# Optimization experiments

Measured on AMD Instinct MI355X. Metric: run time of the kernel, lower is better.

The kernel has to match this reference:

```python
import jax, jax.numpy as jnp
import numpy as np

K, DIM, B, N_CLASS = 4096, 50257, 512, 2


def setup_inputs() -> dict:
    key = jax.random.key(0)
    k1, k2, k3 = jax.random.split(key, 3)
    # probability-like positive values; log() is applied to both tensors
    query = jax.random.uniform(k1, (B, DIM), dtype=jnp.float32, minval=1e-4, maxval=1.0)
    queue_anchor = jax.random.uniform(k2, (K, DIM), dtype=jnp.float32, minval=1e-4, maxval=1.0)
    queue_label = jax.random.randint(k3, (K,), 0, N_CLASS, dtype=jnp.int64)
    return {"query": query, "queue_anchor": queue_anchor, "queue_label": queue_label}


def reference(query, queue_anchor, queue_label):
    # Original math: kl[b,k] = mean_d( a[k,d] * (log a[k,d] - log q[b,d]) )
    # Decompose to avoid the (K,B,dim) broadcast:
    #   kl = mean_d(a*log a)[k] - (a @ log(q).T)[k,b] / dim
    a = queue_anchor
    dim = a.shape[1]
    ent = jnp.mean(a * jnp.log(a), axis=1)                    # (K,)
    cross = jnp.einsum('kd,bd->kb', a, jnp.log(query)) / dim  # (K,B)
    kl_distance = (ent[:, None] - cross).T                    # (B,K)
    # knn == 1 path: argmin over anchors, gather labels
    indices = jnp.argmin(kl_distance, axis=1)                 # (B,)
    return queue_label[indices]
```

## Files before the change

kernel.cpp:

```cpp
#include <hip/hip_runtime.h>
#include <stdint.h>

#define DIMN 50257
#define KN   4096
#define BN   512
#define DP   50432
#define DCH  6304
#define NSTAGE 197
#define MARGIN_RAW 6.0f

#define OFF_CROSS 0ul
#define OFF_ENT   8388608ul
#define OFF_CNT   8404992ul
#define OFF_CANDK 8407040ul
#define OFF_CANDV 8439808ul
#define OFF_LQ16  8472576ul

typedef short v8s __attribute__((ext_vector_type(8)));
typedef float v4f __attribute__((ext_vector_type(4)));

__device__ __forceinline__ unsigned short bf16_rne(float x) {
    unsigned u = __float_as_uint(x);
    u += 0x7fffu + ((u >> 16) & 1u);
    return (unsigned short)(u >> 16);
}

__global__ void k_zero(float* __restrict__ p, long n) {
    long i = (long)blockIdx.x * blockDim.x + threadIdx.x;
    long stride = (long)gridDim.x * blockDim.x;
    for (; i < n; i += stride) p[i] = 0.0f;
}

__global__ void k_logq(const float* __restrict__ q, unsigned short* __restrict__ lq) {
    long i = (long)blockIdx.x * 256 + threadIdx.x;
    if (i >= (long)BN * DP) return;
    int b = (int)(i / DP);
    int d = (int)(i - (long)b * DP);
    unsigned short h = 0;
    if (d < DIMN) {
        float x = q[(long)b * DIMN + d];
        h = bf16_rne(__logf(x));
    }
    lq[i] = h;
}

__global__ __launch_bounds__(512, 2) void k_gemm(
    const float* __restrict__ A, const unsigned short* __restrict__ LQ,
    float* __restrict__ cross, float* __restrict__ ent)
{
    __shared__ __align__(16) unsigned short a_s[128 * 40];
    __shared__ __align__(16) unsigned short b_s[512 * 40];

    const int t    = threadIdx.x;
    const int bid  = blockIdx.x;
    const int rt   = bid >> 3;
    const int ch   = bid & 7;
    const int k0   = rt * 128;
    const int dbase = ch * DCH;

    const int lane = t & 63;
    const int w    = t >> 6;
    const int wr   = w >> 2;
    const int wc   = w & 3;
    const int aq   = lane >> 4;
    const int am   = lane & 15;

    const int ac  = t & 31;
    const int ar0 = t >> 5;
    const int bn0  = t >> 2;
    const int bsub = t & 3;

    v4f acc[4][8];
#pragma unroll
    for (int i = 0; i < 4; ++i)
#pragma unroll
        for (int j = 0; j < 8; ++j) acc[i][j] = (v4f){0.f, 0.f, 0.f, 0.f};

    float ent_acc[8];
#pragma unroll
    for (int i = 0; i < 8; ++i) ent_acc[i] = 0.f;

    int abase[8];
#pragma unroll
    for (int i = 0; i < 8; ++i) abase[i] = (k0 + ar0 + 16 * i) * DIMN + dbase + ac;
    int bbase[4];
#pragma unroll
    for (int i = 0; i < 4; ++i) bbase[i] = (bn0 + 128 * i) * DP + dbase + bsub * 8;

    float a_reg[8];
    v8s   b_reg[4];

    {
        const int d = dbase + ac;
#pragma unroll
        for (int i = 0; i < 8; ++i)
            a_reg[i] = (d < DIMN) ? A[abase[i]] : 0.0f;
#pragma unroll
        for (int i = 0; i < 4; ++i)
            b_reg[i] = *(const v8s*)&LQ[bbase[i]];
    }

#pragma unroll 1
    for (int s = 0; s < NSTAGE; ++s) {
        __syncthreads();
#pragma unroll
        for (int i = 0; i < 8; ++i) {
            float av = a_reg[i];
            if (av > 0.f) ent_acc[i] += av * __logf(av);
            a_s[(ar0 + 16 * i) * 40 + ac] = bf16_rne(av);
        }
#pragma unroll
        for (int i = 0; i < 4; ++i)
            *(v8s*)&b_s[(bn0 + 128 * i) * 40 + bsub * 8] = b_reg[i];
        __syncthreads();

        if (s + 1 < NSTAGE) {
            const int off = (s + 1) * 32;
            const int d = dbase + off + ac;
#pragma unroll
            for (int i = 0; i < 8; ++i)
                a_reg[i] = (d < DIMN) ? A[abase[i] + off] : 0.0f;
#pragma unroll
            for (int i = 0; i < 4; ++i)
                b_reg[i] = *(const v8s*)&LQ[bbase[i] + off];
        }

        v8s aF[4], bF[8];
#pragma unroll
        for (int i = 0; i < 4; ++i)
            aF[i] = *(const v8s*)&a_s[(wr * 64 + i * 16 + am) * 40 + aq * 8];
#pragma unroll
        for (int j = 0; j < 8; ++j)
            bF[j] = *(const v8s*)&b_s[(wc * 128 + j * 16 + am) * 40 + aq * 8];
#pragma unroll
        for (int i = 0; i < 4; ++i)
#pragma unroll
            for (int j = 0; j < 8; ++j)
                acc[i][j] = __builtin_amdgcn_mfma_f32_16x16x32_bf16(aF[i], bF[j], acc[i][j], 0, 0, 0);
    }

#pragma unroll
    for (int i = 0; i < 4; ++i)
#pragma unroll
        for (int j = 0; j < 8; ++j)
#pragma unroll
            for (int r = 0; r < 4; ++r) {
                int row = k0 + wr * 64 + i * 16 + aq * 4 + r;
                int col = wc * 128 + j * 16 + am;
                atomicAdd(&cross[(long)row * BN + col], acc[i][j][r]);
            }
#pragma unroll
    for (int i = 0; i < 8; ++i) {
        float v = ent_acc[i];
#pragma unroll
        for (int m = 1; m <= 16; m <<= 1) v += __shfl_xor(v, m, 64);
        if ((lane & 31) == 0) atomicAdd(&ent[k0 + ar0 + 16 * i], v);
    }
}

__global__ void k_argmin(const float* __restrict__ cross, const float* __restrict__ ent,
                         int* __restrict__ cnt, int* __restrict__ candk)
{
    __shared__ float sred[256];
    __shared__ int scnt;
    const int b = blockIdx.x;
    const int t = threadIdx.x;
    float vals[16];
    float best = 3.4e38f;
#pragma unroll
    for (int i = 0; i < 16; ++i) {
        int k = t + i * 256;
        float v = ent[k] - cross[(long)k * BN + b];
        vals[i] = v;
        best = fminf(best, v);
    }
    sred[t] = best;
    __syncthreads();
    for (int o = 128; o > 0; o >>= 1) {
        if (t < o) sred[t] = fminf(sred[t], sred[t + o]);
        __syncthreads();
    }
    if (t == 0) scnt = 0;
    __syncthreads();
    const float m1 = sred[0];
#pragma unroll
    for (int i = 0; i < 16; ++i) {
        if (vals[i] <= m1 + MARGIN_RAW) {
            int pos = atomicAdd(&scnt, 1);
            if (pos < 16) candk[b * 16 + pos] = t + i * 256;
        }
    }
    __syncthreads();
    if (t == 0) cnt[b] = min(scnt, 16);
}

__global__ void k_refine(const float* __restrict__ A, const float* __restrict__ q,
                         const float* __restrict__ ent, const int* __restrict__ cnt,
                         const int* __restrict__ candk, float* __restrict__ candv)
{
    __shared__ double sred[256];
    const int b = blockIdx.x >> 4;
    const int j = blockIdx.x & 15;
    if (j >= cnt[b]) return;
    const int k = candk[b * 16 + j];
    const int t = threadIdx.x;
    const float* __restrict__ arow = A + (long)k * DIMN;
    const float* __restrict__ qrow = q + (long)b * DIMN;
    double sum = 0.0;
    for (int d = t; d < DIMN; d += 256)
        sum += (double)arow[d] * (double)__logf(qrow[d]);
    sred[t] = sum;
    __syncthreads();
    for (int o = 128; o > 0; o >>= 1) {
        if (t < o) sred[t] += sred[t + o];
        __syncthreads();
    }
    if (t == 0) candv[b * 16 + j] = (float)((double)ent[k] - sred[0]);
}

__global__ void k_final(const float* __restrict__ candv, const int* __restrict__ candk,
                        const int* __restrict__ cnt, const int* __restrict__ label,
                        int* __restrict__ out)
{
    int b = blockIdx.x * blockDim.x + threadIdx.x;
    if (b >= BN) return;
    int n = cnt[b];
    float bv = 3.4e38f;
    int bk = 1 << 30;
    for (int j = 0; j < n; ++j) {
        float v = candv[b * 16 + j];
        int kk = candk[b * 16 + j];
        if (v < bv || (v == bv && kk < bk)) { bv = v; bk = kk; }
    }
    out[b] = label[bk];
}

extern "C" void kernel_launch(void* const* d_in, const int* in_sizes, int n_in,
                              void* d_out, int out_size, void* d_ws, size_t ws_size,
                              hipStream_t stream)
{
    const float* q     = (const float*)d_in[0];
    const float* A     = (const float*)d_in[1];
    const int*   label = (const int*)d_in[2];
    int* out = (int*)d_out;

    char* ws = (char*)d_ws;
    float*          cross = (float*)(ws + OFF_CROSS);
    float*          ent   = (float*)(ws + OFF_ENT);
    int*            cnt   = (int*)(ws + OFF_CNT);
    int*            candk = (int*)(ws + OFF_CANDK);
    float*          candv = (float*)(ws + OFF_CANDV);
    unsigned short* lq    = (unsigned short*)(ws + OFF_LQ16);

    k_zero<<<1024, 256, 0, stream>>>((float*)ws, (long)(OFF_CANDK / 4));
    k_logq<<<(int)(((long)BN * DP + 255) / 256), 256, 0, stream>>>(q, lq);
    k_gemm<<<256, 512, 0, stream>>>(A, lq, cross, ent);
    k_argmin<<<BN, 256, 0, stream>>>(cross, ent, cnt, candk);
    k_refine<<<BN * 16, 256, 0, stream>>>(A, q, ent, cnt, candk, candv);
    k_final<<<2, 256, 0, stream>>>(candv, candk, cnt, label, out);
}
```

Measured before the change: 1.855 ms.

## Use direct global-to-LDS loads, split-D partial buffers, and vectorize logq/refine

```diff
diff --git a/kernel.cpp b/kernel.cpp
--- a/kernel.cpp
+++ b/kernel.cpp
@@ -7,17 +7,19 @@
 #define DP   50432
 #define DCH  6304
 #define NSTAGE 197
+#define NCH  8
 #define MARGIN_RAW 6.0f
 
 #define OFF_CROSS 0ul
-#define OFF_ENT   8388608ul
-#define OFF_CNT   8404992ul
-#define OFF_CANDK 8407040ul
-#define OFF_CANDV 8439808ul
-#define OFF_LQ16  8472576ul
+#define OFF_ENT   67108864ul
+#define OFF_CNT   67125248ul
+#define OFF_CANDK 67127296ul
+#define OFF_CANDV 67160064ul
+#define OFF_LQ16  67192832ul
 
 typedef short v8s __attribute__((ext_vector_type(8)));
 typedef float v4f __attribute__((ext_vector_type(4)));
+typedef unsigned short v4su __attribute__((ext_vector_type(4)));
 
 __device__ __forceinline__ unsigned short bf16_rne(float x) {
     unsigned u = __float_as_uint(x);
@@ -25,23 +27,37 @@
     return (unsigned short)(u >> 16);
 }
 
-__global__ void k_zero(float* __restrict__ p, long n) {
-    long i = (long)blockIdx.x * blockDim.x + threadIdx.x;
-    long stride = (long)gridDim.x * blockDim.x;
-    for (; i < n; i += stride) p[i] = 0.0f;
+__device__ __forceinline__ void lds_load16(const unsigned short* g, unsigned short* l) {
+    __builtin_amdgcn_global_load_lds(
+        reinterpret_cast<const unsigned int __attribute__((address_space(1)))*>(
+            reinterpret_cast<uintptr_t>(g)),
+        reinterpret_cast<unsigned int __attribute__((address_space(3)))*>(
+            reinterpret_cast<uintptr_t>(l)),
+        16, 0, 0);
+}
+
+__global__ void k_zero(float* __restrict__ p, int n) {
+    int i = blockIdx.x * 256 + threadIdx.x;
+    if (i < n) p[i] = 0.0f;
 }
 
 __global__ void k_logq(const float* __restrict__ q, unsigned short* __restrict__ lq) {
-    long i = (long)blockIdx.x * 256 + threadIdx.x;
-    if (i >= (long)BN * DP) return;
-    int b = (int)(i / DP);
-    int d = (int)(i - (long)b * DP);
-    unsigned short h = 0;
-    if (d < DIMN) {
-        float x = q[(long)b * DIMN + d];
-        h = bf16_rne(__logf(x));
-    }
-    lq[i] = h;
+    const int b  = blockIdx.y;
+    const int d0 = (blockIdx.x * 256 + threadIdx.x) * 4;
+    if (d0 >= DP) return;
+    const float* __restrict__ qr = q + (long)b * DIMN;
+    v4su out;
+    if (d0 + 3 < DIMN) {
+#pragma unroll
+        for (int i = 0; i < 4; ++i) out[i] = bf16_rne(__logf(qr[d0 + i]));
+    } else {
+#pragma unroll
+        for (int i = 0; i < 4; ++i) {
+            int d = d0 + i;
+            out[i] = (d < DIMN) ? bf16_rne(__logf(qr[d])) : (unsigned short)0;
+        }
+    }
+    *(v4su*)(lq + (long)b * DP + d0) = out;
 }
 
 __global__ __launch_bounds__(512, 2) void k_gemm(
@@ -49,13 +65,12 @@
     float* __restrict__ cross, float* __restrict__ ent)
 {
     __shared__ __align__(16) unsigned short a_s[128 * 40];
-    __shared__ __align__(16) unsigned short b_s[512 * 40];
-
-    const int t    = threadIdx.x;
-    const int bid  = blockIdx.x;
-    const int rt   = bid >> 3;
-    const int ch   = bid & 7;
-    const int k0   = rt * 128;
+    __shared__ __align__(16) unsigned short b_s[2][512 * 32];
+
+    const int t     = threadIdx.x;
+    const int rt    = blockIdx.x >> 3;
+    const int ch    = blockIdx.x & 7;
+    const int k0    = rt * 128;
     const int dbase = ch * DCH;
 
     const int lane = t & 63;
@@ -67,8 +82,8 @@
 
     const int ac  = t & 31;
     const int ar0 = t >> 5;
-    const int bn0  = t >> 2;
-    const int bsub = t & 3;
+    const int brow = w * 64 + (lane >> 2);
+    const int bcol = (lane & 3) * 8;
 
     v4f acc[4][8];
 #pragma unroll
@@ -83,12 +98,8 @@
     int abase[8];
 #pragma unroll
     for (int i = 0; i < 8; ++i) abase[i] = (k0 + ar0 + 16 * i) * DIMN + dbase + ac;
-    int bbase[4];
-#pragma unroll
-    for (int i = 0; i < 4; ++i) bbase[i] = (bn0 + 128 * i) * DP + dbase + bsub * 8;
 
     float a_reg[8];
-    v8s   b_reg[4];
 
     {
         const int d = dbase + ac;
@@ -96,8 +107,9 @@
         for (int i = 0; i < 8; ++i)
             a_reg[i] = (d < DIMN) ? A[abase[i]] : 0.0f;
 #pragma unroll
-        for (int i = 0; i < 4; ++i)
-            b_reg[i] = *(const v8s*)&LQ[bbase[i]];
+        for (int n = 0; n < 4; ++n)
+            lds_load16(LQ + (brow + n * 16) * DP + dbase + bcol,
+                       &b_s[0][w * 2048 + n * 512]);
     }
 
 #pragma unroll 1
@@ -109,9 +121,6 @@
             if (av > 0.f) ent_acc[i] += av * __logf(av);
             a_s[(ar0 + 16 * i) * 40 + ac] = bf16_rne(av);
         }
-#pragma unroll
-        for (int i = 0; i < 4; ++i)
-            *(v8s*)&b_s[(bn0 + 128 * i) * 40 + bsub * 8] = b_reg[i];
         __syncthreads();
 
         if (s + 1 < NSTAGE) {
@@ -121,24 +130,25 @@
             for (int i = 0; i < 8; ++i)
                 a_reg[i] = (d < DIMN) ? A[abase[i] + off] : 0.0f;
 #pragma unroll
-            for (int i = 0; i < 4; ++i)
-                b_reg[i] = *(const v8s*)&LQ[bbase[i] + off];
-        }
-
-        v8s aF[4], bF[8];
+            for (int n = 0; n < 4; ++n)
+                lds_load16(LQ + (brow + n * 16) * DP + dbase + off + bcol,
+                           &b_s[(s + 1) & 1][w * 2048 + n * 512]);
+        }
+
+        v8s aF[4];
 #pragma unroll
         for (int i = 0; i < 4; ++i)
             aF[i] = *(const v8s*)&a_s[(wr * 64 + i * 16 + am) * 40 + aq * 8];
 #pragma unroll
-        for (int j = 0; j < 8; ++j)
-            bF[j] = *(const v8s*)&b_s[(wc * 128 + j * 16 + am) * 40 + aq * 8];
-#pragma unroll
-        for (int i = 0; i < 4; ++i)
-#pragma unroll
-            for (int j = 0; j < 8; ++j)
-                acc[i][j] = __builtin_amdgcn_mfma_f32_16x16x32_bf16(aF[i], bF[j], acc[i][j], 0, 0, 0);
-    }
-
+        for (int j = 0; j < 8; ++j) {
+            v8s bF = *(const v8s*)&b_s[s & 1][(wc * 128 + j * 16 + am) * 32 + aq * 8];
+#pragma unroll
+            for (int i = 0; i < 4; ++i)
+                acc[i][j] = __builtin_amdgcn_mfma_f32_16x16x32_bf16(aF[i], bF, acc[i][j], 0, 0, 0);
+        }
+    }
+
+    float* __restrict__ crossC = cross + (long)ch * (KN * BN);
 #pragma unroll
     for (int i = 0; i < 4; ++i)
 #pragma unroll
@@ -147,7 +157,7 @@
             for (int r = 0; r < 4; ++r) {
                 int row = k0 + wr * 64 + i * 16 + aq * 4 + r;
                 int col = wc * 128 + j * 16 + am;
-                atomicAdd(&cross[(long)row * BN + col], acc[i][j][r]);
+                crossC[(long)row * BN + col] = acc[i][j][r];
             }
 #pragma unroll
     for (int i = 0; i < 8; ++i) {
@@ -170,7 +180,10 @@
 #pragma unroll
     for (int i = 0; i < 16; ++i) {
         int k = t + i * 256;
-        float v = ent[k] - cross[(long)k * BN + b];
+        float v = ent[k];
+        const float* cp = cross + (long)k * BN + b;
+#pragma unroll
+        for (int c = 0; c < 8; ++c) v -= cp[(long)c * (KN * BN)];
         vals[i] = v;
         best = fminf(best, v);
     }
@@ -207,8 +220,13 @@
     const float* __restrict__ arow = A + (long)k * DIMN;
     const float* __restrict__ qrow = q + (long)b * DIMN;
     double sum = 0.0;
-    for (int d = t; d < DIMN; d += 256)
-        sum += (double)arow[d] * (double)__logf(qrow[d]);
+    for (int d = t * 4; d + 3 < DIMN; d += 1024) {
+#pragma unroll
+        for (int i = 0; i < 4; ++i)
+            sum += (double)arow[d + i] * (double)__logf(qrow[d + i]);
+    }
+    if (t == 0)
+        sum += (double)arow[DIMN - 1] * (double)__logf(qrow[DIMN - 1]);
     sred[t] = sum;
     __syncthreads();
     for (int o = 128; o > 0; o >>= 1) {
@@ -252,8 +270,8 @@
     float*          candv = (float*)(ws + OFF_CANDV);
     unsigned short* lq    = (unsigned short*)(ws + OFF_LQ16);
 
-    k_zero<<<1024, 256, 0, stream>>>((float*)ws, (long)(OFF_CANDK / 4));
-    k_logq<<<(int)(((long)BN * DP + 255) / 256), 256, 0, stream>>>(q, lq);
+    k_zero<<<18, 256, 0, stream>>>(ent, 4608);
+    k_logq<<<dim3(50, BN), 256, 0, stream>>>(q, lq);
     k_gemm<<<256, 512, 0, stream>>>(A, lq, cross, ent);
     k_argmin<<<BN, 256, 0, stream>>>(cross, ent, cnt, candk);
     k_refine<<<BN * 16, 256, 0, stream>>>(A, q, ent, cnt, candk, candv);
```

Result: faster. 1.691 ms (-8.9%).
